# Optimization experiments

Measured on AMD Instinct MI355X. Metric: run time of the kernel, lower is better.

The kernel has to match this reference:

```python
import jax, jax.numpy as jnp
import numpy as np
import math

B, S, HID, H = 4, 4096, 1024, 16
DH = HID // H  # 64

def setup_inputs() -> dict:
    key = jax.random.key(0)
    ks = jax.random.split(key, 6)
    query = jax.random.normal(ks[0], (B, S, HID), dtype=jnp.float32)
    key_t = jax.random.normal(ks[1], (B, S, HID), dtype=jnp.float32)
    value = jax.random.normal(ks[2], (B, S, HID), dtype=jnp.float32)
    attn_mask = jax.random.normal(ks[3], (B, S, H, H), dtype=jnp.float32)
    # nn.Linear(hidden, 3*hidden): weight (3H, H), bias (3H,)
    W_qkv = jax.random.normal(ks[4], (3 * HID, HID), dtype=jnp.float32) * (1.0 / math.sqrt(HID))
    b_qkv = jax.random.normal(ks[5], (3 * HID,), dtype=jnp.float32) * 0.01
    return {"query": query, "key": key_t, "value": value, "attn_mask": attn_mask,
            "W_qkv": W_qkv, "b_qkv": b_qkv}

def reference(query, key, value, attn_mask, W_qkv, b_qkv):
    # fused QKV projection (only `query` is used, matching the source)
    qkv = jnp.einsum('bsh,oh->bso', query, W_qkv) + b_qkv  # (B,S,3*HID)
    q, k, v = jnp.split(qkv, 3, axis=-1)
    q = q.reshape(B, S, H, DH)
    k = k.reshape(B, S, H, DH)
    v = v.reshape(B, S, H, DH)
    # NOTE: no (B,H,S,D) permute in the source -> scores are head-vs-head per position
    scale = 1.0 / math.sqrt(DH)
    qk = jnp.einsum('bshd,bsgd->bshg', q, k) * scale + attn_mask  # (B,S,H,H)
    attn_weight = jax.nn.softmax(qk, axis=-1)
    # dropout_p=0 (eval): identity
    o = jnp.einsum('bshg,bsgd->bshd', attn_weight, v)  # (B,S,H,DH)
    return o.reshape(B, S, HID)
```

## Files before the change

kernel.cpp:

```cpp
#include <hip/hip_runtime.h>
#include <cstdint>
#include <cstddef>


typedef __attribute__((ext_vector_type(8))) short bf16x8;
typedef __attribute__((ext_vector_type(4))) short bf16x4;
typedef __attribute__((ext_vector_type(4))) float f32x4;

__device__ inline unsigned short f2bf(float f) {
  unsigned int i = __float_as_uint(f);
  i += 0x7fff + ((i >> 16) & 1);
  return (unsigned short)(i >> 16);
}

__device__ inline void async16(const void* g, void* l) {
  __builtin_amdgcn_global_load_lds(
      (const __attribute__((address_space(1))) void*)g,
      (__attribute__((address_space(3))) void*)l, 16, 0, 0);
}

__global__ __launch_bounds__(256) void cast2_kernel(const float* __restrict__ in0,
                                                    unsigned short* __restrict__ out0,
                                                    int n0,
                                                    const float* __restrict__ in1,
                                                    unsigned short* __restrict__ out1,
                                                    int n1) {
  int i = (blockIdx.x * 256 + threadIdx.x) * 4;
  const float* src; unsigned short* dst;
  if (i < n0) { src = in0 + i; dst = out0 + i; }
  else {
    int j = i - n0;
    if (j >= n1) return;
    src = in1 + j; dst = out1 + j;
  }
  float4 v = *(const float4*)src;
  union { unsigned short u[4]; unsigned long long ll; } o;
  o.u[0] = f2bf(v.x); o.u[1] = f2bf(v.y); o.u[2] = f2bf(v.z); o.u[3] = f2bf(v.w);
  *(unsigned long long*)dst = o.ll;
}

#define GK 1024
#define GN 3072
__global__ __launch_bounds__(512, 2) void gemm_qkv(const unsigned short* __restrict__ A,
                                                   const unsigned short* __restrict__ Bm,
                                                   const float* __restrict__ bias,
                                                   unsigned short* __restrict__ C) {
  __shared__ unsigned short As[2][256][64];
  __shared__ unsigned short Bs[2][256][64];

  const int bid = blockIdx.x;
  const int swz = (bid & 7) * 96 + (bid >> 3);
  const int m0 = (swz / 12) * 256;
  const int n0 = (swz % 12) * 256;

  const int tid  = threadIdx.x;
  const int lane = tid & 63;
  const int wave = tid >> 6;
  const int wm = wave & 1;
  const int wn = wave >> 1;
  const int fr = lane & 15;
  const int fq = lane >> 4;

  const int r0 = tid >> 3;
  const int c0 = (tid & 7) ^ (r0 & 7);
  const unsigned short* gA = A  + (size_t)(m0 + r0) * GK + c0 * 8;
  const unsigned short* gB = Bm + (size_t)(n0 + r0) * GK + c0 * 8;
  const int ls0 = wave * 512;

#define STAGE_A(tt, hh) do {                                                   \
    unsigned short* lb_ = &As[(tt) & 1][(hh) * 128][0];                        \
    const unsigned short* g_ = gA + (size_t)(hh) * 128 * GK + (tt) * 64;       \
    async16(g_, lb_ + ls0);                                                    \
    async16(g_ + (size_t)64 * GK, lb_ + 4096 + ls0);                           \
  } while (0)
#define STAGE_B(tt, hh) do {                                                   \
    unsigned short* lb_ = &Bs[(tt) & 1][(hh) * 128][0];                        \
    const unsigned short* g_ = gB + (size_t)(hh) * 128 * GK + (tt) * 64;       \
    async16(g_, lb_ + ls0);                                                    \
    async16(g_ + (size_t)64 * GK, lb_ + 4096 + ls0);                           \
  } while (0)

  f32x4 acc[8][4] = {};

  STAGE_A(0, 0); STAGE_A(0, 1); STAGE_B(0, 0); STAGE_B(0, 1);
  STAGE_B(1, 0); STAGE_A(1, 0); STAGE_B(1, 1);

  for (int t = 0; t < 16; ++t) {
    const int cur = t & 1;
    if (t == 0)       { asm volatile("s_waitcnt vmcnt(6)" ::: "memory"); }
    else if (t == 15) { asm volatile("s_waitcnt vmcnt(0)" ::: "memory"); }
    else              { asm volatile("s_waitcnt vmcnt(8)" ::: "memory"); }
    __builtin_amdgcn_s_barrier();
    __builtin_amdgcn_sched_barrier(0);

    bf16x8 bfr[4][2];
    #pragma unroll
    for (int p = 0; p < 4; ++p) {
      bf16x8 af[2][2];
      #pragma unroll
      for (int ii = 0; ii < 2; ++ii) {
        const int rA = (p * 2 + ii) * 32 + wm * 16 + fr;
        #pragma unroll
        for (int ks = 0; ks < 2; ++ks)
          af[ii][ks] = *(const bf16x8*)&As[cur][rA][((ks * 4 + fq) ^ (rA & 7)) * 8];
      }
      if (p == 0) {
        #pragma unroll
        for (int j = 0; j < 4; ++j) {
          const int rB = wn * 64 + j * 16 + fr;
          #pragma unroll
          for (int ks = 0; ks < 2; ++ks)
            bfr[j][ks] = *(const bf16x8*)&Bs[cur][rB][((ks * 4 + fq) ^ (rB & 7)) * 8];
        }
        if (t + 1 < 16) { STAGE_A(t + 1, 1); }
      }
      if (p == 1) {
        asm volatile("s_waitcnt vmcnt(8)" ::: "memory");
      }
      if (p == 2 && t + 2 < 16) { STAGE_B(t + 2, 0); }
      if (p == 3 && t + 2 < 16) { STAGE_A(t + 2, 0); STAGE_B(t + 2, 1); }

      __builtin_amdgcn_s_barrier();
      __builtin_amdgcn_sched_barrier(0);
      __builtin_amdgcn_s_setprio(1);
      #pragma unroll
      for (int ks = 0; ks < 2; ++ks)
        #pragma unroll
        for (int ii = 0; ii < 2; ++ii)
          #pragma unroll
          for (int j = 0; j < 4; ++j)
            acc[p * 2 + ii][j] = __builtin_amdgcn_mfma_f32_16x16x32_bf16(
                af[ii][ks], bfr[j][ks], acc[p * 2 + ii][j], 0, 0, 0);
      __builtin_amdgcn_s_setprio(0);
      __builtin_amdgcn_sched_barrier(0);
    }
  }
#undef STAGE_A
#undef STAGE_B

  #pragma unroll
  for (int i = 0; i < 8; ++i) {
    #pragma unroll
    for (int j = 0; j < 4; ++j) {
      const int col = n0 + wn * 64 + j * 16 + fr;
      const float bc = bias[col];
      const int rowb = m0 + i * 32 + wm * 16 + fq * 4;
      #pragma unroll
      for (int rr = 0; rr < 4; ++rr)
        C[(size_t)(rowb + rr) * GN + col] = f2bf(acc[i][j][rr] + bc);
    }
  }
}

__global__ __launch_bounds__(256) void attn_kernel(const unsigned short* __restrict__ QKV,
                                                   const float* __restrict__ mask,
                                                   float* __restrict__ out) {
  __shared__ unsigned short shV[4][1024];
  const int wave = threadIdx.x >> 6;
  const int lane = threadIdx.x & 63;
  const int pos = blockIdx.x * 4 + wave;

  const unsigned short* row = QKV + (size_t)pos * 3072;

  async16(&row[2048 + (size_t)lane * 8], &shV[wave][0]);
  async16(&row[2048 + 512 + (size_t)lane * 8], &shV[wave][512]);

  const int hn  = lane & 15;
  const int grp = lane >> 4;

  const int qk_off = hn * 64 + grp * 8;
  bf16x8 qf0 = *(const bf16x8*)&row[qk_off];
  bf16x8 qf1 = *(const bf16x8*)&row[qk_off + 32];
  bf16x8 kf0 = *(const bf16x8*)&row[1024 + qk_off];
  bf16x8 kf1 = *(const bf16x8*)&row[1024 + qk_off + 32];

  float4 mk = *(const float4*)&mask[(size_t)pos * 256 + hn * 16 + grp * 4];

  f32x4 s = {};
  s = __builtin_amdgcn_mfma_f32_16x16x32_bf16(kf0, qf0, s, 0, 0, 0);
  s = __builtin_amdgcn_mfma_f32_16x16x32_bf16(kf1, qf1, s, 0, 0, 0);

  float sv0 = s[0] * 0.125f + mk.x;
  float sv1 = s[1] * 0.125f + mk.y;
  float sv2 = s[2] * 0.125f + mk.z;
  float sv3 = s[3] * 0.125f + mk.w;
  float mx = fmaxf(fmaxf(sv0, sv1), fmaxf(sv2, sv3));
  mx = fmaxf(mx, __shfl_xor(mx, 16));
  mx = fmaxf(mx, __shfl_xor(mx, 32));
  float p0 = __expf(sv0 - mx), p1 = __expf(sv1 - mx);
  float p2 = __expf(sv2 - mx), p3 = __expf(sv3 - mx);
  float sum = p0 + p1 + p2 + p3;
  sum += __shfl_xor(sum, 16);
  sum += __shfl_xor(sum, 32);
  const float inv = 1.f / sum;

  union { unsigned u[2]; bf16x4 v; } pa;
  pa.u[0] = (unsigned)f2bf(p0 * inv) | ((unsigned)f2bf(p1 * inv) << 16);
  pa.u[1] = (unsigned)f2bf(p2 * inv) | ((unsigned)f2bf(p3 * inv) << 16);

  asm volatile("s_waitcnt vmcnt(0)" ::: "memory");

  const unsigned short* vb = &shV[wave][grp * 256];
  #pragma unroll
  for (int db = 0; db < 4; ++db) {
    const int e0 = db * 16 + hn;
    unsigned v0 = vb[e0], v1 = vb[e0 + 64], v2 = vb[e0 + 128], v3 = vb[e0 + 192];
    union { unsigned u[2]; bf16x4 v; } bfv;
    bfv.u[0] = v0 | (v1 << 16);
    bfv.u[1] = v2 | (v3 << 16);
    f32x4 z = {};
#if __has_builtin(__builtin_amdgcn_mfma_f32_16x16x16bf16_1k)
    f32x4 o4 = __builtin_amdgcn_mfma_f32_16x16x16bf16_1k(bfv.v, pa.v, z, 0, 0, 0);
    *(float4*)(out + (size_t)pos * 1024 + hn * 64 + db * 16 + grp * 4) =
        *(const float4*)&o4;
#else
    const int src = grp * 32 + hn;
    unsigned a0 = __shfl((int)pa.u[0], src), a1 = __shfl((int)pa.u[1], src);
    unsigned a2 = __shfl((int)pa.u[0], src + 16), a3 = __shfl((int)pa.u[1], src + 16);
    if (grp >= 2) { a0 = a1 = a2 = a3 = 0; }
    union { unsigned u[4]; bf16x8 v; } paw;
    paw.u[0] = a0; paw.u[1] = a1; paw.u[2] = a2; paw.u[3] = a3;
    const unsigned short* vbf = &shV[wave][((grp & 1) * 8) * 64];
    unsigned w0 = vbf[e0],       w1 = vbf[e0 + 64],  w2 = vbf[e0 + 128], w3 = vbf[e0 + 192];
    unsigned w4 = vbf[e0 + 256], w5 = vbf[e0 + 320], w6 = vbf[e0 + 384], w7 = vbf[e0 + 448];
    union { unsigned u[4]; bf16x8 v; } bfw;
    bfw.u[0] = w0 | (w1 << 16); bfw.u[1] = w2 | (w3 << 16);
    bfw.u[2] = w4 | (w5 << 16); bfw.u[3] = w6 | (w7 << 16);
    f32x4 o4 = __builtin_amdgcn_mfma_f32_16x16x32_bf16(paw.v, bfw.v, z, 0, 0, 0);
    #pragma unroll
    for (int r = 0; r < 4; ++r)
      out[(size_t)pos * 1024 + (grp * 4 + r) * 64 + db * 16 + hn] = o4[r];
#endif
  }
}

extern "C" void kernel_launch(void* const* d_in, const int* in_sizes, int n_in,
                              void* d_out, int out_size, void* d_ws, size_t ws_size,
                              hipStream_t stream) {
  const float* query = (const float*)d_in[0];
  const float* mask  = (const float*)d_in[3];
  const float* Wqkv  = (const float*)d_in[4];
  const float* bqkv  = (const float*)d_in[5];
  float* out = (float*)d_out;

  unsigned short* qb   = (unsigned short*)d_ws;
  unsigned short* wb   = (unsigned short*)((char*)d_ws + 33554432);
  unsigned short* qkvb = (unsigned short*)((char*)d_ws + 39845888);

  cast2_kernel<<<19456, 256, 0, stream>>>(query, qb, 16777216, Wqkv, wb, 3145728);

  gemm_qkv<<<768, 512, 0, stream>>>(qb, wb, bqkv, qkvb);

  attn_kernel<<<4096, 256, 0, stream>>>(qkvb, mask, out);
}
```

Measured before the change: 315.9 us.

## Split QKV GEMM into three launches and use 16x16x32 MFMA in attention

Splits the single 768-block QKV GEMM launch into three 256-block launches using a block-offset parameter. Replaces the attention PV step's 16x16x16 MFMA path with a 16x16x32 bf16 MFMA whose probability operand is built once by lane shuffles with zero padding, hoisted out of the loop. It also adds a min-blocks occupancy hint to the attention kernel. The extra launches add overhead and barriers between GEMM chunks. Half of each K=32 MFMA multiplies zeros.

```diff
diff --git a/kernel.cpp b/kernel.cpp
--- a/kernel.cpp
+++ b/kernel.cpp
@@ -44,11 +44,12 @@
 __global__ __launch_bounds__(512, 2) void gemm_qkv(const unsigned short* __restrict__ A,
                                                    const unsigned short* __restrict__ Bm,
                                                    const float* __restrict__ bias,
-                                                   unsigned short* __restrict__ C) {
+                                                   unsigned short* __restrict__ C,
+                                                   int base) {
   __shared__ unsigned short As[2][256][64];
   __shared__ unsigned short Bs[2][256][64];
 
-  const int bid = blockIdx.x;
+  const int bid = base + blockIdx.x;
   const int swz = (bid & 7) * 96 + (bid >> 3);
   const int m0 = (swz / 12) * 256;
   const int n0 = (swz % 12) * 256;
@@ -152,9 +153,9 @@
   }
 }
 
-__global__ __launch_bounds__(256) void attn_kernel(const unsigned short* __restrict__ QKV,
-                                                   const float* __restrict__ mask,
-                                                   float* __restrict__ out) {
+__global__ __launch_bounds__(256, 4) void attn_kernel(const unsigned short* __restrict__ QKV,
+                                                      const float* __restrict__ mask,
+                                                      float* __restrict__ out) {
   __shared__ unsigned short shV[4][1024];
   const int wave = threadIdx.x >> 6;
   const int lane = threadIdx.x & 63;
@@ -198,39 +199,30 @@
   pa.u[0] = (unsigned)f2bf(p0 * inv) | ((unsigned)f2bf(p1 * inv) << 16);
   pa.u[1] = (unsigned)f2bf(p2 * inv) | ((unsigned)f2bf(p3 * inv) << 16);
 
+  const int src = grp * 32 + hn;
+  unsigned b0 = __shfl((int)pa.u[0], src),      b1 = __shfl((int)pa.u[1], src);
+  unsigned b2 = __shfl((int)pa.u[0], src + 16), b3 = __shfl((int)pa.u[1], src + 16);
+  if (grp >= 2) { b0 = b1 = b2 = b3 = 0; }
+  union { unsigned u[4]; bf16x8 v; } pb;
+  pb.u[0] = b0; pb.u[1] = b1; pb.u[2] = b2; pb.u[3] = b3;
+
   asm volatile("s_waitcnt vmcnt(0)" ::: "memory");
 
-  const unsigned short* vb = &shV[wave][grp * 256];
+  const unsigned short* va = &shV[wave][(grp & 1) * 8 * 64];
   #pragma unroll
   for (int db = 0; db < 4; ++db) {
     const int e0 = db * 16 + hn;
-    unsigned v0 = vb[e0], v1 = vb[e0 + 64], v2 = vb[e0 + 128], v3 = vb[e0 + 192];
-    union { unsigned u[2]; bf16x4 v; } bfv;
-    bfv.u[0] = v0 | (v1 << 16);
-    bfv.u[1] = v2 | (v3 << 16);
+    union { unsigned u[4]; bf16x8 v; } av;
+    #pragma unroll
+    for (int jj = 0; jj < 4; ++jj) {
+      unsigned lo = va[(2 * jj) * 64 + e0];
+      unsigned hi = va[(2 * jj + 1) * 64 + e0];
+      av.u[jj] = lo | (hi << 16);
+    }
     f32x4 z = {};
-#if __has_builtin(__builtin_amdgcn_mfma_f32_16x16x16bf16_1k)
-    f32x4 o4 = __builtin_amdgcn_mfma_f32_16x16x16bf16_1k(bfv.v, pa.v, z, 0, 0, 0);
+    f32x4 o4 = __builtin_amdgcn_mfma_f32_16x16x32_bf16(av.v, pb.v, z, 0, 0, 0);
     *(float4*)(out + (size_t)pos * 1024 + hn * 64 + db * 16 + grp * 4) =
         *(const float4*)&o4;
-#else
-    const int src = grp * 32 + hn;
-    unsigned a0 = __shfl((int)pa.u[0], src), a1 = __shfl((int)pa.u[1], src);
-    unsigned a2 = __shfl((int)pa.u[0], src + 16), a3 = __shfl((int)pa.u[1], src + 16);
-    if (grp >= 2) { a0 = a1 = a2 = a3 = 0; }
-    union { unsigned u[4]; bf16x8 v; } paw;
-    paw.u[0] = a0; paw.u[1] = a1; paw.u[2] = a2; paw.u[3] = a3;
-    const unsigned short* vbf = &shV[wave][((grp & 1) * 8) * 64];
-    unsigned w0 = vbf[e0],       w1 = vbf[e0 + 64],  w2 = vbf[e0 + 128], w3 = vbf[e0 + 192];
-    unsigned w4 = vbf[e0 + 256], w5 = vbf[e0 + 320], w6 = vbf[e0 + 384], w7 = vbf[e0 + 448];
-    union { unsigned u[4]; bf16x8 v; } bfw;
-    bfw.u[0] = w0 | (w1 << 16); bfw.u[1] = w2 | (w3 << 16);
-    bfw.u[2] = w4 | (w5 << 16); bfw.u[3] = w6 | (w7 << 16);
-    f32x4 o4 = __builtin_amdgcn_mfma_f32_16x16x32_bf16(paw.v, bfw.v, z, 0, 0, 0);
-    #pragma unroll
-    for (int r = 0; r < 4; ++r)
-      out[(size_t)pos * 1024 + (grp * 4 + r) * 64 + db * 16 + hn] = o4[r];
-#endif
   }
 }
 
@@ -249,7 +241,9 @@
 
   cast2_kernel<<<19456, 256, 0, stream>>>(query, qb, 16777216, Wqkv, wb, 3145728);
 
-  gemm_qkv<<<768, 512, 0, stream>>>(qb, wb, bqkv, qkvb);
+  gemm_qkv<<<256, 512, 0, stream>>>(qb, wb, bqkv, qkvb, 0);
+  gemm_qkv<<<256, 512, 0, stream>>>(qb, wb, bqkv, qkvb, 256);
+  gemm_qkv<<<256, 512, 0, stream>>>(qb, wb, bqkv, qkvb, 512);
 
   attn_kernel<<<4096, 256, 0, stream>>>(qkvb, mask, out);
 }
```

Measured after the change: 320.2 us. About the same (+1.4%).
